# Kernel optimization log

Hardware: AMD Instinct MI355X
Metric: run time of the kernel (lower is better)

The kernel has to match this reference:

```python
import jax, jax.numpy as jnp
import numpy as np


def setup_inputs() -> dict:
    key = jax.random.key(0)
    k1, k2, k3 = jax.random.split(key, 3)
    N, E, D_IN, D_OUT = 100000, 1600000, 64, 64
    x = jax.random.normal(k1, (N, D_IN), dtype=jnp.float32)
    edge_index = jax.random.randint(k2, (2, E), 0, N, dtype=jnp.int64)
    # Glorot-style init for the GCN weight, zero bias (PyG defaults)
    W = jax.random.normal(k3, (D_IN, D_OUT), dtype=jnp.float32) * (1.0 / np.sqrt(D_IN))
    b = jnp.zeros((D_OUT,), dtype=jnp.float32)
    return {"x": x, "edge_index": edge_index, "W": W, "b": b}


def reference(x, edge_index, W, b):
    # GCNConv (PyG semantics, add_self_loops=True, normalize=True) followed by
    # Dropout (eval mode -> identity) and ReLU.
    N = x.shape[0]
    # Linear transform first (small GEMM)
    xw = x @ W  # [N, D_OUT]
    # Add self-loops
    loops = jnp.arange(N, dtype=edge_index.dtype)
    row = jnp.concatenate([edge_index[0], loops])  # source nodes
    col = jnp.concatenate([edge_index[1], loops])  # destination nodes
    # Symmetric degree normalization: deg over destination index (PyG gcn_norm)
    ones = jnp.ones(col.shape[0], dtype=xw.dtype)
    deg = jax.ops.segment_sum(ones, col, num_segments=N)
    deg_inv_sqrt = jnp.where(deg > 0, jax.lax.rsqrt(deg), 0.0)
    norm = deg_inv_sqrt[row] * deg_inv_sqrt[col]  # [E+N]
    # Gather source features, scale, scatter-add to destinations
    msgs = norm[:, None] * xw[row]  # [E+N, D_OUT]
    out = jax.ops.segment_sum(msgs, col, num_segments=N)
    out = out + b
    # dropout in eval mode is identity
    return jax.nn.relu(out)
```

## Files before the change

kernel.cpp:

```cpp
#include <hip/hip_runtime.h>
#include <hip/hip_fp16.h>


#define D 64
#define BW 256
#define CAPB 4800
#define CAPL 2944
#define EPT 16
#define PART_T 512
#define EPB (PART_T * EPT)
#define NBMAX 512
#define GSTRIDE 16

typedef __attribute__((ext_vector_type(8))) short bf16x8;
typedef __attribute__((ext_vector_type(4))) float f32x4;

__device__ __forceinline__ unsigned short f2bf(float f) {
    unsigned u = __float_as_uint(f);
    u += 0x7FFFu + ((u >> 16) & 1u);
    return (unsigned short)(u >> 16);
}

__global__ __launch_bounds__(512)
void k_part(const int* __restrict__ row, const int* __restrict__ col,
            int* __restrict__ gcur, int* __restrict__ dense,
            unsigned short* __restrict__ WT, const float* __restrict__ W,
            unsigned short* __restrict__ xw_h,
            int E, int NBUCK, int N) {
    __shared__ int lh[NBMAX];
    __shared__ int lst[NBMAX + 1];
    __shared__ int bas[NBMAX];
    __shared__ int wsc[8];
    __shared__ int srtv[EPB];
    int tid = threadIdx.x;
    for (int i = tid; i < NBUCK; i += PART_T) lh[i] = 0;
    __syncthreads();
    int e0 = blockIdx.x * EPB + tid;
    int rr[EPT], cc[EPT], pp[EPT];
#pragma unroll
    for (int i = 0; i < EPT; ++i) {
        int e = e0 + i * PART_T;
        if (e < E) {
            cc[i] = __builtin_nontemporal_load(col + e);
            rr[i] = __builtin_nontemporal_load(row + e);
            pp[i] = atomicAdd(&lh[cc[i] >> 8], 1);
        } else {
            cc[i] = -1;
        }
    }
    __syncthreads();
    int rot = (int)((blockIdx.x * 97u) % (unsigned)NBUCK);
    for (int j = tid; j < NBUCK; j += PART_T) {
        int bu = j + rot; if (bu >= NBUCK) bu -= NBUCK;
        int h = lh[bu];
        if (h > 0) bas[bu] = atomicAdd(&gcur[bu * GSTRIDE], h);
    }
    int lane = tid & 63, wv = tid >> 6;
    int v = (tid < NBUCK) ? lh[tid] : 0;
    int inc = v;
#pragma unroll
    for (int o = 1; o < 64; o <<= 1) {
        int u = __shfl_up(inc, o);
        if (lane >= o) inc += u;
    }
    if (lane == 63) wsc[wv] = inc;
    __syncthreads();
    int woff = 0;
#pragma unroll
    for (int w = 0; w < 8; ++w) woff += (w < wv) ? wsc[w] : 0;
    if (tid < NBUCK) lst[tid] = woff + inc - v;
    int tot = min(EPB, E - blockIdx.x * EPB);
    if (tid == 0) lst[NBUCK] = tot;
    __syncthreads();
#pragma unroll
    for (int i = 0; i < EPT; ++i) {
        if (cc[i] >= 0)
            srtv[lst[cc[i] >> 8] + pp[i]] = (rr[i] << 8) | (cc[i] & 255);
    }
    __syncthreads();
    for (int p = tid; p < tot; p += PART_T) {
        int lo = 0, hi = NBUCK;
        while (hi - lo > 1) {
            int mid = (lo + hi) >> 1;
            if (lst[mid] <= p) lo = mid; else hi = mid;
        }
        int gpos = bas[lo] + (p - lst[lo]);
        if (gpos < CAPB) dense[(size_t)lo * CAPB + gpos] = srtv[p];
    }
    if (blockIdx.x == 0) {
        for (int i = tid; i < 4096; i += PART_T) {
            int n = i >> 6, k = i & 63;
            WT[i] = f2bf(W[k * 64 + n]);
        }
        if (tid < 32) ((unsigned*)xw_h)[(size_t)N * 32 + tid] = 0u;
    }
}

__global__ __launch_bounds__(256, 4)
void k_gemm(const float* __restrict__ x, const unsigned short* __restrict__ WT,
            const int* __restrict__ dense, const int* __restrict__ gcur,
            unsigned char* __restrict__ deg8, unsigned short* __restrict__ xw_h,
            int N, int NT) {
    __shared__ int lh[BW];
    int tid = threadIdx.x, b = blockIdx.x;
    lh[tid] = 0;
    __syncthreads();
    int tot = min(gcur[b * GSTRIDE], CAPB);
    const int* dn = dense + (size_t)b * CAPB;
    for (int i = tid; i < tot; i += 256)
        atomicAdd(&lh[__builtin_nontemporal_load(dn + i) & 255], 1);
    __syncthreads();
    {
        int node = b * BW + tid;
        if (node < N) deg8[node] = (unsigned char)min(lh[tid], 255);
    }
    int lane = tid & 63, wv = tid >> 6;
    int m = lane & 15, quad = lane >> 4;
    bf16x8 Bf[4][2];
#pragma unroll
    for (int t = 0; t < 4; ++t)
#pragma unroll
        for (int s = 0; s < 2; ++s)
            Bf[t][s] = *(const bf16x8*)(WT + (t * 16 + m) * 64 + s * 32 + quad * 8);
#pragma unroll
    for (int s = 0; s < 4; ++s) {
        int mt = b * 16 + s * 4 + wv;
        if (mt >= NT) continue;
        int row0 = mt * 16;
        const float* xr = x + (size_t)(row0 + m) * 64 + quad * 8;
        f32x4 a0 = __builtin_nontemporal_load((const f32x4*)(xr));
        f32x4 a1 = __builtin_nontemporal_load((const f32x4*)(xr + 4));
        f32x4 a2 = __builtin_nontemporal_load((const f32x4*)(xr + 32));
        f32x4 a3 = __builtin_nontemporal_load((const f32x4*)(xr + 36));
        bf16x8 A0, A1;
        A0[0] = (short)f2bf(a0[0]); A0[1] = (short)f2bf(a0[1]);
        A0[2] = (short)f2bf(a0[2]); A0[3] = (short)f2bf(a0[3]);
        A0[4] = (short)f2bf(a1[0]); A0[5] = (short)f2bf(a1[1]);
        A0[6] = (short)f2bf(a1[2]); A0[7] = (short)f2bf(a1[3]);
        A1[0] = (short)f2bf(a2[0]); A1[1] = (short)f2bf(a2[1]);
        A1[2] = (short)f2bf(a2[2]); A1[3] = (short)f2bf(a2[3]);
        A1[4] = (short)f2bf(a3[0]); A1[5] = (short)f2bf(a3[1]);
        A1[6] = (short)f2bf(a3[2]); A1[7] = (short)f2bf(a3[3]);
        f32x4 acc[4];
#pragma unroll
        for (int t = 0; t < 4; ++t) {
            acc[t] = (f32x4){0.f, 0.f, 0.f, 0.f};
            acc[t] = __builtin_amdgcn_mfma_f32_16x16x32_bf16(Bf[t][0], A0, acc[t], 0, 0, 0);
            acc[t] = __builtin_amdgcn_mfma_f32_16x16x32_bf16(Bf[t][1], A1, acc[t], 0, 0, 0);
        }
        float dsc = rsqrtf((float)(lh[(row0 + m) & 255] + 1));
        unsigned short* op = xw_h + (size_t)(row0 + m) * 64 + quad * 4;
#pragma unroll
        for (int t = 0; t < 4; ++t) {
            __half2 h0, h1;
            h0.x = __float2half(acc[t][0] * dsc); h0.y = __float2half(acc[t][1] * dsc);
            h1.x = __float2half(acc[t][2] * dsc); h1.y = __float2half(acc[t][3] * dsc);
            uint2 u; u.x = *(unsigned*)&h0; u.y = *(unsigned*)&h1;
            *(uint2*)(op + t * 16) = u;
        }
    }
}

__global__ __launch_bounds__(512, 2)
void k_gather(const int* __restrict__ dense, const int* __restrict__ gcur,
              const unsigned char* __restrict__ deg8,
              const uint2* __restrict__ xwh, const float* __restrict__ bias,
              float* __restrict__ out, int* __restrict__ tick,
              int N, int NBUCK) {
    __shared__ int lh[128], stt[128], cur[128];
    __shared__ int wsum[2];
    __shared__ int sb;
    __shared__ __align__(16) int srtL[CAPL];
    int tid = threadIdx.x, lane = tid & 63;
    int l = lane & 15;
    int ng = lane >> 4;
    int wv = tid >> 6;
    const float4 bb = ((const float4*)bias)[l];
#define ADDV(h)                                                     \
    {                                                               \
        __half2 h0 = *(__half2*)&(h).x, h1 = *(__half2*)&(h).y;     \
        float2 f0 = __half22float2(h0), f1 = __half22float2(h1);    \
        acc.x += f0.x; acc.y += f0.y; acc.z += f1.x; acc.w += f1.y; \
    }
    while (true) {
        if (tid == 0) sb = atomicAdd(tick, 1);
        __syncthreads();
        int t = sb;
        if (t >= 2 * NBUCK) break;
        int b = t >> 1, hf = t & 1;
        int nb0 = b * BW + hf * 128;
        int v = 0, vp = 0, inc = 0;
        if (tid < 128) {
            int node = nb0 + tid;
            v = (node < N) ? (int)deg8[node] : 0;
            lh[tid] = v;
            vp = (v + 3) & ~3; inc = vp;
#pragma unroll
            for (int o = 1; o < 64; o <<= 1) {
                int u = __shfl_up(inc, o);
                if (lane >= o) inc += u;
            }
            if (lane == 63) wsum[tid >> 6] = inc;
        }
        __syncthreads();
        if (tid < 128) {
            int st = inc - vp + ((tid >> 6) ? wsum[0] : 0);
            stt[tid] = st;
            cur[tid] = st;
        }
        __syncthreads();
        int tot = min(gcur[b * GSTRIDE], CAPB);
        const int* dn = dense + (size_t)b * CAPB;
        int hsel = hf << 7;
        for (int i = tid; i < tot; i += 512) {
            int val = __builtin_nontemporal_load(dn + i);
            if ((val & 128) == hsel) {
                int pos = atomicAdd(&cur[val & 127], 1);
                if (pos < CAPL) srtL[pos] = val >> 8;
            }
        }
        __syncthreads();
        if (tid < 128) {
            int e = stt[tid] + v, ep = min(stt[tid] + vp, CAPL);
            for (; e < ep; ++e) srtL[e] = N;
        }
        __syncthreads();
#pragma unroll
        for (int g = 0; g < 4; ++g) {
            int nn = g * 32 + wv * 4 + ng;
            int node = nb0 + nn;
            bool active = node < N;
            float4 acc = make_float4(0.f, 0.f, 0.f, 0.f);
            int k = 0, s0 = 0;
            if (active) {
                k = lh[nn]; s0 = stt[nn];
                uint2 hs = xwh[(size_t)node * 16 + l];
                ADDV(hs);
            }
            int kp = (k + 3) & ~3;
            if (s0 + kp > CAPL) kp = (CAPL > s0) ? ((CAPL - s0) & ~3) : 0;
            if (kp > 0) {
                int4 rv = *(const int4*)&srtL[s0];
                uint2 va = xwh[(size_t)rv.x * 16 + l];
                uint2 vb = xwh[(size_t)rv.y * 16 + l];
                uint2 vc = xwh[(size_t)rv.z * 16 + l];
                uint2 vd = xwh[(size_t)rv.w * 16 + l];
                for (int j = 4; j < kp; j += 4) {
                    int4 r2 = *(const int4*)&srtL[s0 + j];
                    uint2 wa = xwh[(size_t)r2.x * 16 + l];
                    uint2 wb = xwh[(size_t)r2.y * 16 + l];
                    uint2 wc = xwh[(size_t)r2.z * 16 + l];
                    uint2 wd = xwh[(size_t)r2.w * 16 + l];
                    ADDV(va); ADDV(vb); ADDV(vc); ADDV(vd);
                    va = wa; vb = wb; vc = wc; vd = wd;
                }
                ADDV(va); ADDV(vb); ADDV(vc); ADDV(vd);
            }
            if (active) {
                float dn2 = rsqrtf((float)(k + 1));
                f32x4 o;
                o[0] = fmaxf(fmaf(dn2, acc.x, bb.x), 0.f);
                o[1] = fmaxf(fmaf(dn2, acc.y, bb.y), 0.f);
                o[2] = fmaxf(fmaf(dn2, acc.z, bb.z), 0.f);
                o[3] = fmaxf(fmaf(dn2, acc.w, bb.w), 0.f);
                __builtin_nontemporal_store(o, (f32x4*)(out + ((size_t)node * 16 + l) * 4));
            }
        }
        __syncthreads();
    }
#undef ADDV
}

extern "C" void kernel_launch(void* const* d_in, const int* in_sizes, int n_in,
                              void* d_out, int out_size, void* d_ws, size_t ws_size,
                              hipStream_t stream) {
    const float* x    = (const float*)d_in[0];
    const int*   ei   = (const int*)d_in[1];
    const float* W    = (const float*)d_in[2];
    const float* bias = (const float*)d_in[3];
    float* out = (float*)d_out;

    const int N = in_sizes[0] / D;
    const int E = in_sizes[1] / 2;
    const int* row = ei;
    const int* col = ei + E;

    const int NBUCK = (N + BW - 1) / BW;
    const int NB1   = (E + EPB - 1) / EPB;
    const int NT    = (N + 15) / 16;

    char* ws = (char*)d_ws;
    size_t o = 0;
    unsigned short* xw_h = (unsigned short*)(ws + o);
    o += (size_t)(N + 1) * D * sizeof(unsigned short);
    int* dense = (int*)(ws + o); o += (size_t)NBUCK * CAPB * sizeof(int);
    int* gcur  = (int*)(ws + o); o += (size_t)NBUCK * GSTRIDE * sizeof(int);
    int* tick  = (int*)(ws + o); o += 16 * sizeof(int);
    unsigned char* deg8 = (unsigned char*)(ws + o); o += (size_t)N;
    o = (o + 15) & ~(size_t)15;
    unsigned short* WT = (unsigned short*)(ws + o); o += 4096 * sizeof(unsigned short);

    hipMemsetAsync(gcur, 0, ((size_t)NBUCK * GSTRIDE + 16) * sizeof(int), stream);
    k_part<<<NB1, PART_T, 0, stream>>>(row, col, gcur, dense, WT, W, xw_h, E, NBUCK, N);
    k_gemm<<<NBUCK, 256, 0, stream>>>(x, WT, dense, gcur, deg8, xw_h, N, NT);
    k_gather<<<512, 512, 0, stream>>>(dense, gcur, deg8, (const uint2*)xw_h,
                                      bias, out, tick, N, NBUCK);
}
```

Measured before the change: 175.3 us.

## Replace persistent half-bucket gather with one 1024-thread block per bucket and wave-per-node

The gather kernel drops the atomic-ticket persistent loop over half-buckets and launches one 1024-thread block per 256-node bucket, sorting the whole bucket's edges into a larger LDS buffer in a single pass. Each wave now handles 16 consecutive nodes one at a time, with the four 16-lane groups splitting a node's neighbours and combining partial sums through cross-lane shuffles. Padding moves from multiples of 4 to multiples of 16. The aim is to avoid filtering the dense edge list twice and to spread high-degree nodes over more lanes, at the cost of more padding work, extra shuffle reductions, larger LDS use that may lower occupancy, and no dynamic load balancing.

```diff
diff --git a/kernel.cpp b/kernel.cpp
--- a/kernel.cpp
+++ b/kernel.cpp
@@ -5,7 +5,7 @@
 #define D 64
 #define BW 256
 #define CAPB 4800
-#define CAPL 2944
+#define CAPL 6912
 #define EPT 16
 #define PART_T 512
 #define EPB (PART_T * EPT)
@@ -161,19 +161,53 @@
     }
 }
 
-__global__ __launch_bounds__(512, 2)
+__global__ __launch_bounds__(1024, 8)
 void k_gather(const int* __restrict__ dense, const int* __restrict__ gcur,
               const unsigned char* __restrict__ deg8,
               const uint2* __restrict__ xwh, const float* __restrict__ bias,
-              float* __restrict__ out, int* __restrict__ tick,
-              int N, int NBUCK) {
-    __shared__ int lh[128], stt[128], cur[128];
-    __shared__ int wsum[2];
-    __shared__ int sb;
+              float* __restrict__ out, int N) {
+    __shared__ int lh[BW], stt[BW], cur[BW];
+    __shared__ int wsum[4];
     __shared__ __align__(16) int srtL[CAPL];
-    int tid = threadIdx.x, lane = tid & 63;
+    int b = blockIdx.x, tid = threadIdx.x, lane = tid & 63;
+    int v = 0, vp = 0, inc = 0;
+    if (tid < BW) {
+        int node = b * BW + tid;
+        v = (node < N) ? (int)deg8[node] : 0;
+        lh[tid] = v;
+        vp = (v + 15) & ~15; inc = vp;
+#pragma unroll
+        for (int o = 1; o < 64; o <<= 1) {
+            int u = __shfl_up(inc, o);
+            if (lane >= o) inc += u;
+        }
+        if (lane == 63) wsum[tid >> 6] = inc;
+    }
+    __syncthreads();
+    if (tid < BW) {
+        int wv4 = tid >> 6, woff = 0;
+#pragma unroll
+        for (int w = 0; w < 4; ++w) woff += (w < wv4) ? wsum[w] : 0;
+        int st = woff + inc - vp;
+        stt[tid] = st;
+        cur[tid] = st;
+    }
+    __syncthreads();
+    int tot = min(gcur[b * GSTRIDE], CAPB);
+    const int* dn = dense + (size_t)b * CAPB;
+    for (int i = tid; i < tot; i += 1024) {
+        int val = __builtin_nontemporal_load(dn + i);
+        int pos = atomicAdd(&cur[val & 255], 1);
+        if (pos < CAPL) srtL[pos] = val >> 8;
+    }
+    __syncthreads();
+    if (tid < BW) {
+        int e = stt[tid] + v, ep = min(stt[tid] + vp, CAPL);
+        for (; e < ep; ++e) srtL[e] = N;
+    }
+    __syncthreads();
+    int q = lane >> 4;
     int l = lane & 15;
-    int ng = lane >> 4;
     int wv = tid >> 6;
     const float4 bb = ((const float4*)bias)[l];
 #define ADDV(h)                                                     \
@@ -182,91 +216,47 @@
         float2 f0 = __half22float2(h0), f1 = __half22float2(h1);    \
         acc.x += f0.x; acc.y += f0.y; acc.z += f1.x; acc.w += f1.y; \
     }
-    while (true) {
-        if (tid == 0) sb = atomicAdd(tick, 1);
-        __syncthreads();
-        int t = sb;
-        if (t >= 2 * NBUCK) break;
-        int b = t >> 1, hf = t & 1;
-        int nb0 = b * BW + hf * 128;
-        int v = 0, vp = 0, inc = 0;
-        if (tid < 128) {
-            int node = nb0 + tid;
-            v = (node < N) ? (int)deg8[node] : 0;
-            lh[tid] = v;
-            vp = (v + 3) & ~3; inc = vp;
-#pragma unroll
-            for (int o = 1; o < 64; o <<= 1) {
-                int u = __shfl_up(inc, o);
-                if (lane >= o) inc += u;
+    for (int nn = wv * 16; nn < wv * 16 + 16; ++nn) {
+        int node = b * BW + nn;
+        if (node >= N) break;
+        int k = lh[nn], s0 = stt[nn];
+        int kp = (k + 15) & ~15;
+        if (s0 + kp > CAPL) kp = (CAPL > s0) ? ((CAPL - s0) & ~15) : 0;
+        float4 acc = make_float4(0.f, 0.f, 0.f, 0.f);
+        if (q == 0) { uint2 hs = xwh[(size_t)node * 16 + l]; ADDV(hs); }
+        int rounds = kp >> 4;
+        if (rounds > 0) {
+            int i0 = s0 + q;
+            int r0 = srtL[i0], r1 = srtL[i0 + 4], r2 = srtL[i0 + 8], r3 = srtL[i0 + 12];
+            uint2 va = xwh[(size_t)r0 * 16 + l];
+            uint2 vb = xwh[(size_t)r1 * 16 + l];
+            uint2 vc = xwh[(size_t)r2 * 16 + l];
+            uint2 vd = xwh[(size_t)r3 * 16 + l];
+            for (int r = 1; r < rounds; ++r) {
+                i0 += 16;
+                int s0n = srtL[i0], s1n = srtL[i0 + 4], s2n = srtL[i0 + 8], s3n = srtL[i0 + 12];
+                uint2 wa = xwh[(size_t)s0n * 16 + l];
+                uint2 wb = xwh[(size_t)s1n * 16 + l];
+                uint2 wc = xwh[(size_t)s2n * 16 + l];
+                uint2 wd = xwh[(size_t)s3n * 16 + l];
+                ADDV(va); ADDV(vb); ADDV(vc); ADDV(vd);
+                va = wa; vb = wb; vc = wc; vd = wd;
             }
-            if (lane == 63) wsum[tid >> 6] = inc;
-        }
-        __syncthreads();
-        if (tid < 128) {
-            int st = inc - vp + ((tid >> 6) ? wsum[0] : 0);
-            stt[tid] = st;
-            cur[tid] = st;
-        }
-        __syncthreads();
-        int tot = min(gcur[b * GSTRIDE], CAPB);
-        const int* dn = dense + (size_t)b * CAPB;
-        int hsel = hf << 7;
-        for (int i = tid; i < tot; i += 512) {
-            int val = __builtin_nontemporal_load(dn + i);
-            if ((val & 128) == hsel) {
-                int pos = atomicAdd(&cur[val & 127], 1);
-                if (pos < CAPL) srtL[pos] = val >> 8;
-            }
-        }
-        __syncthreads();
-        if (tid < 128) {
-            int e = stt[tid] + v, ep = min(stt[tid] + vp, CAPL);
-            for (; e < ep; ++e) srtL[e] = N;
-        }
-        __syncthreads();
-#pragma unroll
-        for (int g = 0; g < 4; ++g) {
-            int nn = g * 32 + wv * 4 + ng;
-            int node = nb0 + nn;
-            bool active = node < N;
-            float4 acc = make_float4(0.f, 0.f, 0.f, 0.f);
-            int k = 0, s0 = 0;
-            if (active) {
-                k = lh[nn]; s0 = stt[nn];
-                uint2 hs = xwh[(size_t)node * 16 + l];
-                ADDV(hs);
-            }
-            int kp = (k + 3) & ~3;
-            if (s0 + kp > CAPL) kp = (CAPL > s0) ? ((CAPL - s0) & ~3) : 0;
-            if (kp > 0) {
-                int4 rv = *(const int4*)&srtL[s0];
-                uint2 va = xwh[(size_t)rv.x * 16 + l];
-                uint2 vb = xwh[(size_t)rv.y * 16 + l];
-                uint2 vc = xwh[(size_t)rv.z * 16 + l];
-                uint2 vd = xwh[(size_t)rv.w * 16 + l];
-                for (int j = 4; j < kp; j += 4) {
-                    int4 r2 = *(const int4*)&srtL[s0 + j];
-                    uint2 wa = xwh[(size_t)r2.x * 16 + l];
-                    uint2 wb = xwh[(size_t)r2.y * 16 + l];
-                    uint2 wc = xwh[(size_t)r2.z * 16 + l];
-                    uint2 wd = xwh[(size_t)r2.w * 16 + l];
-                    ADDV(va); ADDV(vb); ADDV(vc); ADDV(vd);
-                    va = wa; vb = wb; vc = wc; vd = wd;
-                }
-                ADDV(va); ADDV(vb); ADDV(vc); ADDV(vd);
-            }
-            if (active) {
-                float dn2 = rsqrtf((float)(k + 1));
-                f32x4 o;
-                o[0] = fmaxf(fmaf(dn2, acc.x, bb.x), 0.f);
-                o[1] = fmaxf(fmaf(dn2, acc.y, bb.y), 0.f);
-                o[2] = fmaxf(fmaf(dn2, acc.z, bb.z), 0.f);
-                o[3] = fmaxf(fmaf(dn2, acc.w, bb.w), 0.f);
-                __builtin_nontemporal_store(o, (f32x4*)(out + ((size_t)node * 16 + l) * 4));
-            }
-        }
-        __syncthreads();
+            ADDV(va); ADDV(vb); ADDV(vc); ADDV(vd);
+        }
+        acc.x += __shfl_xor(acc.x, 16); acc.y += __shfl_xor(acc.y, 16);
+        acc.z += __shfl_xor(acc.z, 16); acc.w += __shfl_xor(acc.w, 16);
+        acc.x += __shfl_xor(acc.x, 32); acc.y += __shfl_xor(acc.y, 32);
+        acc.z += __shfl_xor(acc.z, 32); acc.w += __shfl_xor(acc.w, 32);
+        if (q == 0) {
+            float dn2 = rsqrtf((float)(k + 1));
+            f32x4 o;
+            o[0] = fmaxf(fmaf(dn2, acc.x, bb.x), 0.f);
+            o[1] = fmaxf(fmaf(dn2, acc.y, bb.y), 0.f);
+            o[2] = fmaxf(fmaf(dn2, acc.z, bb.z), 0.f);
+            o[3] = fmaxf(fmaf(dn2, acc.w, bb.w), 0.f);
+            __builtin_nontemporal_store(o, (f32x4*)(out + ((size_t)node * 16 + l) * 4));
+        }
     }
 #undef ADDV
 }
@@ -295,14 +285,13 @@
     o += (size_t)(N + 1) * D * sizeof(unsigned short);
     int* dense = (int*)(ws + o); o += (size_t)NBUCK * CAPB * sizeof(int);
     int* gcur  = (int*)(ws + o); o += (size_t)NBUCK * GSTRIDE * sizeof(int);
-    int* tick  = (int*)(ws + o); o += 16 * sizeof(int);
     unsigned char* deg8 = (unsigned char*)(ws + o); o += (size_t)N;
     o = (o + 15) & ~(size_t)15;
     unsigned short* WT = (unsigned short*)(ws + o); o += 4096 * sizeof(unsigned short);
 
-    hipMemsetAsync(gcur, 0, ((size_t)NBUCK * GSTRIDE + 16) * sizeof(int), stream);
+    hipMemsetAsync(gcur, 0, (size_t)NBUCK * GSTRIDE * sizeof(int), stream);
     k_part<<<NB1, PART_T, 0, stream>>>(row, col, gcur, dense, WT, W, xw_h, E, NBUCK, N);
     k_gemm<<<NBUCK, 256, 0, stream>>>(x, WT, dense, gcur, deg8, xw_h, N, NT);
-    k_gather<<<512, 512, 0, stream>>>(dense, gcur, deg8, (const uint2*)xw_h,
-                                      bias, out, tick, N, NBUCK);
-}
+    k_gather<<<NBUCK, 1024, 0, stream>>>(dense, gcur, deg8, (const uint2*)xw_h,
+                                         bias, out, N);
+}
```

New measurement: 166.0 us. -5.3%, faster.
